# Kernel optimization log

Hardware: AMD Instinct MI355X
Metric: run time of the kernel (lower is better)

## Reference

```python
import jax, jax.numpy as jnp
import numpy as np

N_HEAD = 16
N_FEAT = 1024
D_HEAD = N_FEAT // N_HEAD


def setup_inputs() -> dict:
    key = jax.random.key(0)
    ks = jax.random.split(key, 12)
    B, L, T = 8, 128, 64
    s = 0.05
    return {
        "q": jax.random.normal(ks[0], (B, 1, N_FEAT), jnp.float32),
        "kv": jax.random.normal(ks[1], (B, L, T, N_FEAT), jnp.float32),
        "Wq": jax.random.normal(ks[2], (D_HEAD, D_HEAD), jnp.float32) * s,
        "bq": jax.random.normal(ks[3], (D_HEAD,), jnp.float32) * s,
        "Wk": jax.random.normal(ks[4], (D_HEAD, D_HEAD), jnp.float32) * s,
        "bk": jax.random.normal(ks[5], (D_HEAD,), jnp.float32) * s,
        "Wv": jax.random.normal(ks[6], (D_HEAD, D_HEAD), jnp.float32) * s,
        "bv": jax.random.normal(ks[7], (D_HEAD,), jnp.float32) * s,
        "Wo": jax.random.normal(ks[8], (N_FEAT, N_FEAT), jnp.float32) * s,
        "bo": jax.random.normal(ks[9], (N_FEAT,), jnp.float32) * s,
    }


def reference(q, kv, Wq, bq, Wk, bk, Wv, bv, Wo, bo):
    B, L, T, D = kv.shape
    H, dh = N_HEAD, D_HEAD
    # mean-pool q over its singleton length dim and kv over T for keys
    qm = q.mean(axis=-2)                      # [B, D]
    km = kv.mean(axis=-2)                     # [B, L, D]
    qh = qm.reshape(B, H, dh)                 # [B, H, dh]
    kh = km.reshape(B, L, H, dh)              # [B, L, H, dh]
    vh = kv.reshape(B, L, T, H, dh)           # [B, L, T, H, dh]
    # per-head linear projections (torch Linear: x @ W.T + b)
    qh = qh @ Wq.T + bq
    kh = kh @ Wk.T + bk
    vh = vh @ Wv.T + bv
    # faithful transpose chain from the original module
    qh = jnp.swapaxes(qh, -2, -3)             # [H, B, dh]  (3D: swaps B and H)
    kh = jnp.swapaxes(kh, -2, -3)             # [B, H, L, dh]
    # broadcasted matmul -> cross-batch attention [B, H, B, L]
    attw = jnp.matmul(qh, jnp.swapaxes(kh, -1, -2)) / jnp.sqrt(jnp.float32(dh))
    attn = jax.nn.softmax(attw, axis=-1)      # [B, H, B, L]
    # value reshuffle: [B,L,T,H,dh] -> [B,H,T,L,dh] -> [B,H,T,dh,L] -> [B,H,T*dh,L]
    v = jnp.swapaxes(vh, -2, -4)
    v = jnp.swapaxes(v, -1, -2)
    v = v.reshape(B, H, T * dh, L)
    ct = jnp.matmul(attn, jnp.swapaxes(v, -1, -2))   # [B, H, B, T*dh]
    ct = ct.reshape(B, H, B, T, dh)
    ct = jnp.swapaxes(ct, -2, -4)                    # [B, T, B, H, dh]
    ct = ct.reshape(B, T, B, H * dh)                 # [B, T, B, D]
    return ct @ Wo.T + bo
```

## Files before the change

### kernel.cpp

```cpp
#include <hip/hip_runtime.h>
#include <hip/hip_bf16.h>

#define BDIM 8
#define LDIM 128
#define TDIM 64
#define NFEAT 1024
#define HNUM 16
#define DH 64

#define GM 4096
#define GN 1024
#define GK 1024

typedef __attribute__((ext_vector_type(8))) short short8;
typedef __attribute__((ext_vector_type(4))) float f32x4;

__device__ __forceinline__ unsigned short f2bf(float x) {
  union { float f; unsigned u; } v; v.f = x;
  unsigned r = v.u + 0x7fffu + ((v.u >> 16) & 1u);
  return (unsigned short)(r >> 16);
}

__device__ __forceinline__ void gload_lds16(const void* g, void* l) {
  __builtin_amdgcn_global_load_lds((const __attribute__((address_space(1))) void*)g,
                                   (__attribute__((address_space(3))) void*)l, 16, 0, 0);
}

__global__ __launch_bounds__(256) void mean_kernel(const float* __restrict__ kv,
                                                   float* __restrict__ km) {
  const int bl = blockIdx.x;
  const float* src = kv + (size_t)bl * (TDIM * NFEAT) + threadIdx.x * 4;
  float4 acc = make_float4(0.f, 0.f, 0.f, 0.f);
#pragma unroll 4
  for (int t = 0; t < TDIM; ++t) {
    const float4 v = *(const float4*)(src + t * NFEAT);
    acc.x += v.x; acc.y += v.y; acc.z += v.z; acc.w += v.w;
  }
  const float s = 1.f / TDIM;
  const float4 o = make_float4(acc.x * s, acc.y * s, acc.z * s, acc.w * s);
  *(float4*)(km + (size_t)bl * NFEAT + threadIdx.x * 4) = o;
}

__global__ __launch_bounds__(128) void attn_kernel(const float* __restrict__ q,
                                                   const float* __restrict__ km,
                                                   const float* __restrict__ Wq,
                                                   const float* __restrict__ bq,
                                                   const float* __restrict__ Wk,
                                                   float* __restrict__ attn) {
  __shared__ float qp_s[BDIM * DH];
  __shared__ float qk_s[BDIM * DH];
  __shared__ float sw[BDIM * LDIM];
  __shared__ float mred[BDIM], ired[BDIM];
  const int b1 = blockIdx.x;
  const int h  = blockIdx.y;
  const int tid = threadIdx.x;

  {
    const int e0 = tid * 4;
    const int b2 = e0 >> 6;
    const int d0 = e0 & 63;
    float a0 = bq[d0], a1 = bq[d0 + 1], a2 = bq[d0 + 2], a3 = bq[d0 + 3];
    const float* qrow = q + b2 * NFEAT + h * DH;
#pragma unroll 4
    for (int i = 0; i < DH; ++i) {
      const float qv = qrow[i];
      a0 += qv * Wq[(d0 + 0) * DH + i];
      a1 += qv * Wq[(d0 + 1) * DH + i];
      a2 += qv * Wq[(d0 + 2) * DH + i];
      a3 += qv * Wq[(d0 + 3) * DH + i];
    }
    qp_s[e0 + 0] = a0; qp_s[e0 + 1] = a1; qp_s[e0 + 2] = a2; qp_s[e0 + 3] = a3;
  }
  __syncthreads();
  {
    const int e0 = tid * 4;
    const int b2 = e0 >> 6;
    const int i0 = e0 & 63;
    float a0 = 0, a1 = 0, a2 = 0, a3 = 0;
#pragma unroll 4
    for (int d = 0; d < DH; ++d) {
      const float qpv = qp_s[b2 * DH + d];
      const float4 wk4 = *(const float4*)(Wk + d * DH + i0);
      a0 += qpv * wk4.x; a1 += qpv * wk4.y; a2 += qpv * wk4.z; a3 += qpv * wk4.w;
    }
    qk_s[e0 + 0] = a0; qk_s[e0 + 1] = a1; qk_s[e0 + 2] = a2; qk_s[e0 + 3] = a3;
  }
  __syncthreads();
  const int l = tid;
  {
    const float* kmrow = km + (size_t)(b1 * LDIM + l) * NFEAT + h * DH;
    float s[8] = {0, 0, 0, 0, 0, 0, 0, 0};
#pragma unroll
    for (int i4 = 0; i4 < DH / 4; ++i4) {
      const float4 kmv = *(const float4*)(kmrow + i4 * 4);
#pragma unroll
      for (int b2 = 0; b2 < 8; ++b2) {
        const float4 qk4 = *(const float4*)(qk_s + b2 * DH + i4 * 4);
        s[b2] += kmv.x * qk4.x + kmv.y * qk4.y + kmv.z * qk4.z + kmv.w * qk4.w;
      }
    }
#pragma unroll
    for (int b2 = 0; b2 < 8; ++b2) sw[b2 * LDIM + l] = s[b2] * 0.125f;
  }
  __syncthreads();
  if (tid < 8) {
    const int b2 = tid;
    float m = -1e30f;
    for (int j = 0; j < LDIM; ++j) m = fmaxf(m, sw[b2 * LDIM + j]);
    float ssum = 0.f;
    for (int j = 0; j < LDIM; ++j) ssum += expf(sw[b2 * LDIM + j] - m);
    mred[b2] = m;
    ired[b2] = 1.f / ssum;
  }
  __syncthreads();
  float* abase = attn + ((size_t)(b1 * HNUM + h) * BDIM) * LDIM + l;
#pragma unroll
  for (int b2 = 0; b2 < 8; ++b2) {
    abase[b2 * LDIM] = expf(sw[b2 * LDIM + l] - mred[b2]) * ired[b2];
  }
}

__global__ __launch_bounds__(256) void weff_kernel(const float* __restrict__ Wo,
                                                   const float* __restrict__ Wv,
                                                   const float* __restrict__ bv,
                                                   const float* __restrict__ bo,
                                                   unsigned short* __restrict__ Weff,
                                                   float* __restrict__ beff) {
  __shared__ float worow[NFEAT];
  __shared__ float red[256];
  const int f = blockIdx.x;
  const int tid = threadIdx.x;
  *(float4*)(worow + tid * 4) = *(const float4*)(Wo + (size_t)f * NFEAT + tid * 4);
  __syncthreads();
  const int g0 = tid * 4;
  const int hbase = (g0 >> 6) << 6;
  const int i0 = g0 & 63;
  float a0 = 0, a1 = 0, a2 = 0, a3 = 0;
#pragma unroll 4
  for (int d = 0; d < DH; ++d) {
    const float wod = worow[hbase + d];
    const float4 wv4 = *(const float4*)(Wv + d * DH + i0);
    a0 += wod * wv4.x; a1 += wod * wv4.y; a2 += wod * wv4.z; a3 += wod * wv4.w;
  }
  ushort4 pk;
  pk.x = f2bf(a0); pk.y = f2bf(a1); pk.z = f2bf(a2); pk.w = f2bf(a3);
  *(ushort4*)(Weff + (size_t)f * NFEAT + g0) = pk;
  red[tid] = worow[g0 + 0] * bv[i0 + 0] + worow[g0 + 1] * bv[i0 + 1] +
             worow[g0 + 2] * bv[i0 + 2] + worow[g0 + 3] * bv[i0 + 3];
  __syncthreads();
  for (int sft = 128; sft > 0; sft >>= 1) {
    if (tid < sft) red[tid] += red[tid + sft];
    __syncthreads();
  }
  if (tid == 0) beff[f] = bo[f] + red[0];
}

__global__ __launch_bounds__(64) void pool_kernel(const float* __restrict__ kv,
                                                  const float* __restrict__ attn,
                                                  unsigned short* __restrict__ pooled) {
  __shared__ float wlds[4 * BDIM * LDIM];
  const int b1 = blockIdx.x;
  const int t = blockIdx.y;
  const int ftile = blockIdx.z;
  const int tid = threadIdx.x;
  {
    const float* src = attn + ((size_t)(b1 * HNUM + ftile * 4)) * (BDIM * LDIM);
#pragma unroll
    for (int j = 0; j < 16; ++j) {
      const int idx = (j * 64 + tid) * 4;
      *(float4*)(wlds + idx) = *(const float4*)(src + idx);
    }
  }
  __syncthreads();
  const int f = ftile * 256 + tid * 4;
  const int hh = tid >> 4;
  const float* kvbase = kv + ((size_t)b1 * LDIM) * (TDIM * NFEAT) + t * NFEAT + f;
  float4 acc[8];
#pragma unroll
  for (int b2 = 0; b2 < 8; ++b2) acc[b2] = make_float4(0.f, 0.f, 0.f, 0.f);
  const float* wbase = wlds + hh * (BDIM * LDIM);
#pragma unroll 2
  for (int l = 0; l < LDIM; ++l) {
    const float4 v = *(const float4*)(kvbase + (size_t)l * (TDIM * NFEAT));
#pragma unroll
    for (int b2 = 0; b2 < 8; ++b2) {
      const float w = wbase[b2 * LDIM + l];
      acc[b2].x += w * v.x; acc[b2].y += w * v.y;
      acc[b2].z += w * v.z; acc[b2].w += w * v.w;
    }
  }
  unsigned short* obase = pooled + ((size_t)(b1 * TDIM + t) * BDIM) * NFEAT + f;
#pragma unroll
  for (int b2 = 0; b2 < 8; ++b2) {
    ushort4 pk;
    pk.x = f2bf(acc[b2].x); pk.y = f2bf(acc[b2].y);
    pk.z = f2bf(acc[b2].z); pk.w = f2bf(acc[b2].w);
    *(ushort4*)(obase + b2 * NFEAT) = pk;
  }
}

__global__ __launch_bounds__(256) void mfma_gemm(const unsigned short* __restrict__ A,
                                                 const unsigned short* __restrict__ W,
                                                 const float* __restrict__ beff,
                                                 float* __restrict__ out) {
  __shared__ unsigned short As[128 * 32];
  __shared__ unsigned short Bs[128 * 32];
  const int tid = threadIdx.x;
  const int w = tid >> 6, l = tid & 63;
  const int mBase = blockIdx.y * 128, nBase = blockIdx.x * 128;
  const int wr = w >> 1, wc = w & 1;

  int sr[2], sc[2];
#pragma unroll
  for (int j = 0; j < 2; ++j) {
    const int o = (w * 2 + j) * 1024 + l * 16;
    const int r = o >> 6;
    const int c = (o >> 4) & 3;
    sr[j] = r;
    sc[j] = (c ^ ((r >> 1) & 3)) * 8;
  }
  const int rl = l & 15, ks = l >> 4;
  const int fsel = (ks ^ ((rl >> 1) & 3)) * 16;
  const int aoff0 = (wr * 64 + rl) * 64 + fsel;
  const int boff0 = (wc * 64 + rl) * 64 + fsel;

  f32x4 acc[4][4] = {};
  for (int k0 = 0; k0 < GK; k0 += 32) {
#pragma unroll
    for (int j = 0; j < 2; ++j) {
      gload_lds16(A + (size_t)(mBase + sr[j]) * GK + k0 + sc[j],
                  (char*)As + (w * 2 + j) * 1024);
      gload_lds16(W + (size_t)(nBase + sr[j]) * GK + k0 + sc[j],
                  (char*)Bs + (w * 2 + j) * 1024);
    }
    __syncthreads();
    short8 a[4], b[4];
#pragma unroll
    for (int m = 0; m < 4; ++m)
      a[m] = *(const short8*)((const char*)As + aoff0 + m * 1024);
#pragma unroll
    for (int n = 0; n < 4; ++n)
      b[n] = *(const short8*)((const char*)Bs + boff0 + n * 1024);
#pragma unroll
    for (int m = 0; m < 4; ++m)
#pragma unroll
      for (int n = 0; n < 4; ++n)
        acc[m][n] = __builtin_amdgcn_mfma_f32_16x16x32_bf16(a[m], b[n], acc[m][n], 0, 0, 0);
    __syncthreads();
  }

#pragma unroll
  for (int n = 0; n < 4; ++n) {
    const int col = nBase + wc * 64 + n * 16 + rl;
    const float bv = beff[col];
#pragma unroll
    for (int m = 0; m < 4; ++m) {
      const int row0 = mBase + wr * 64 + m * 16 + ks * 4;
#pragma unroll
      for (int j2 = 0; j2 < 4; ++j2)
        out[(size_t)(row0 + j2) * GN + col] = acc[m][n][j2] + bv;
    }
  }
}

extern "C" void kernel_launch(void* const* d_in, const int* in_sizes, int n_in,
                              void* d_out, int out_size, void* d_ws, size_t ws_size,
                              hipStream_t stream) {
  const float* q  = (const float*)d_in[0];
  const float* kv = (const float*)d_in[1];
  const float* Wq = (const float*)d_in[2];
  const float* bq = (const float*)d_in[3];
  const float* Wk = (const float*)d_in[4];
  const float* Wv = (const float*)d_in[6];
  const float* bv = (const float*)d_in[7];
  const float* Wo = (const float*)d_in[8];
  const float* bo = (const float*)d_in[9];
  float* out = (float*)d_out;

  char* ws = (char*)d_ws;
  float*          km     = (float*)ws;
  float*          attn   = (float*)(ws + (4u << 20));
  float*          beff   = (float*)(ws + (4u << 20) + (512u << 10));
  unsigned short* Weff   = (unsigned short*)(ws + (4u << 20) + (516u << 10));
  unsigned short* pooled = (unsigned short*)(ws + (4u << 20) + (516u << 10) + (2u << 20));

  mean_kernel<<<BDIM * LDIM, 256, 0, stream>>>(kv, km);
  attn_kernel<<<dim3(BDIM, HNUM), 128, 0, stream>>>(q, km, Wq, bq, Wk, attn);
  weff_kernel<<<NFEAT, 256, 0, stream>>>(Wo, Wv, bv, bo, Weff, beff);
  pool_kernel<<<dim3(BDIM, TDIM, 4), 64, 0, stream>>>(kv, attn, pooled);
  mfma_gemm<<<dim3(GN / 128, GM / 128), 256, 0, stream>>>(pooled, Weff, beff, out);
}
```

Baseline: 153.7 us.

## Batch loads in mean/pool kernels, pad LDS, double-buffer narrower GEMM tiles

```diff
diff --git a/kernel.cpp b/kernel.cpp
--- a/kernel.cpp
+++ b/kernel.cpp
@@ -31,10 +31,14 @@
   const int bl = blockIdx.x;
   const float* src = kv + (size_t)bl * (TDIM * NFEAT) + threadIdx.x * 4;
   float4 acc = make_float4(0.f, 0.f, 0.f, 0.f);
-#pragma unroll 4
-  for (int t = 0; t < TDIM; ++t) {
-    const float4 v = *(const float4*)(src + t * NFEAT);
-    acc.x += v.x; acc.y += v.y; acc.z += v.z; acc.w += v.w;
+  for (int t0 = 0; t0 < TDIM; t0 += 8) {
+    float4 v[8];
+#pragma unroll
+    for (int j = 0; j < 8; ++j) v[j] = *(const float4*)(src + (t0 + j) * NFEAT);
+#pragma unroll
+    for (int j = 0; j < 8; ++j) {
+      acc.x += v[j].x; acc.y += v[j].y; acc.z += v[j].z; acc.w += v[j].w;
+    }
   }
   const float s = 1.f / TDIM;
   const float4 o = make_float4(acc.x * s, acc.y * s, acc.z * s, acc.w * s);
@@ -155,20 +159,24 @@
   if (tid == 0) beff[f] = bo[f] + red[0];
 }
 
+#define HSTRIDE 1032
 __global__ __launch_bounds__(64) void pool_kernel(const float* __restrict__ kv,
                                                   const float* __restrict__ attn,
                                                   unsigned short* __restrict__ pooled) {
-  __shared__ float wlds[4 * BDIM * LDIM];
+  __shared__ float wlds[4 * HSTRIDE];
   const int b1 = blockIdx.x;
   const int t = blockIdx.y;
   const int ftile = blockIdx.z;
   const int tid = threadIdx.x;
   {
-    const float* src = attn + ((size_t)(b1 * HNUM + ftile * 4)) * (BDIM * LDIM);
-#pragma unroll
-    for (int j = 0; j < 16; ++j) {
-      const int idx = (j * 64 + tid) * 4;
-      *(float4*)(wlds + idx) = *(const float4*)(src + idx);
+#pragma unroll
+    for (int hg = 0; hg < 4; ++hg) {
+      const float* src = attn + ((size_t)(b1 * HNUM + ftile * 4 + hg)) * (BDIM * LDIM);
+#pragma unroll
+      for (int j = 0; j < 4; ++j) {
+        const int idx = (j * 64 + tid) * 4;
+        *(float4*)(wlds + hg * HSTRIDE + idx) = *(const float4*)(src + idx);
+      }
     }
   }
   __syncthreads();
@@ -178,15 +186,20 @@
   float4 acc[8];
 #pragma unroll
   for (int b2 = 0; b2 < 8; ++b2) acc[b2] = make_float4(0.f, 0.f, 0.f, 0.f);
-  const float* wbase = wlds + hh * (BDIM * LDIM);
-#pragma unroll 2
-  for (int l = 0; l < LDIM; ++l) {
-    const float4 v = *(const float4*)(kvbase + (size_t)l * (TDIM * NFEAT));
-#pragma unroll
-    for (int b2 = 0; b2 < 8; ++b2) {
-      const float w = wbase[b2 * LDIM + l];
-      acc[b2].x += w * v.x; acc[b2].y += w * v.y;
-      acc[b2].z += w * v.z; acc[b2].w += w * v.w;
+  const float* wbase = wlds + hh * HSTRIDE;
+  for (int l0 = 0; l0 < LDIM; l0 += 8) {
+    float4 v[8];
+#pragma unroll
+    for (int j = 0; j < 8; ++j)
+      v[j] = *(const float4*)(kvbase + (size_t)(l0 + j) * (TDIM * NFEAT));
+#pragma unroll
+    for (int j = 0; j < 8; ++j) {
+#pragma unroll
+      for (int b2 = 0; b2 < 8; ++b2) {
+        const float w = wbase[b2 * LDIM + l0 + j];
+        acc[b2].x += w * v[j].x; acc[b2].y += w * v[j].y;
+        acc[b2].z += w * v[j].z; acc[b2].w += w * v[j].w;
+      }
     }
   }
   unsigned short* obase = pooled + ((size_t)(b1 * TDIM + t) * BDIM) * NFEAT + f;
@@ -203,55 +216,66 @@
                                                  const unsigned short* __restrict__ W,
                                                  const float* __restrict__ beff,
                                                  float* __restrict__ out) {
-  __shared__ unsigned short As[128 * 32];
-  __shared__ unsigned short Bs[128 * 32];
+  __shared__ unsigned short As[2][128 * 32];
+  __shared__ unsigned short Bs[2][64 * 32];
   const int tid = threadIdx.x;
   const int w = tid >> 6, l = tid & 63;
-  const int mBase = blockIdx.y * 128, nBase = blockIdx.x * 128;
+  const int mBase = blockIdx.y * 128, nBase = blockIdx.x * 64;
   const int wr = w >> 1, wc = w & 1;
 
-  int sr[2], sc[2];
+  int arow[2], acol[2];
 #pragma unroll
   for (int j = 0; j < 2; ++j) {
-    const int o = (w * 2 + j) * 1024 + l * 16;
-    const int r = o >> 6;
-    const int c = (o >> 4) & 3;
-    sr[j] = r;
-    sc[j] = (c ^ ((r >> 1) & 3)) * 8;
-  }
+    const int cid = j * 256 + tid;
+    const int r = cid >> 2, c = cid & 3;
+    arow[j] = r;
+    acol[j] = (c ^ ((r >> 1) & 3)) * 8;
+  }
+  const int brow = tid >> 2;
+  const int bcol = ((tid & 3) ^ ((brow >> 1) & 3)) * 8;
+
   const int rl = l & 15, ks = l >> 4;
   const int fsel = (ks ^ ((rl >> 1) & 3)) * 16;
-  const int aoff0 = (wr * 64 + rl) * 64 + fsel;
-  const int boff0 = (wc * 64 + rl) * 64 + fsel;
-
-  f32x4 acc[4][4] = {};
-  for (int k0 = 0; k0 < GK; k0 += 32) {
-#pragma unroll
-    for (int j = 0; j < 2; ++j) {
-      gload_lds16(A + (size_t)(mBase + sr[j]) * GK + k0 + sc[j],
-                  (char*)As + (w * 2 + j) * 1024);
-      gload_lds16(W + (size_t)(nBase + sr[j]) * GK + k0 + sc[j],
-                  (char*)Bs + (w * 2 + j) * 1024);
-    }
-    __syncthreads();
-    short8 a[4], b[4];
+
+  f32x4 acc[4][2] = {};
+
+#pragma unroll
+  for (int j = 0; j < 2; ++j)
+    gload_lds16(A + (size_t)(mBase + arow[j]) * GK + acol[j],
+                (char*)As[0] + (j * 256 + tid) * 16);
+  gload_lds16(W + (size_t)(nBase + brow) * GK + bcol, (char*)Bs[0] + tid * 16);
+  __syncthreads();
+
+  int cur = 0;
+  for (int t = 0; t < GK / 32; ++t) {
+    if (t + 1 < GK / 32) {
+      const int k0 = (t + 1) * 32;
+#pragma unroll
+      for (int j = 0; j < 2; ++j)
+        gload_lds16(A + (size_t)(mBase + arow[j]) * GK + k0 + acol[j],
+                    (char*)As[cur ^ 1] + (j * 256 + tid) * 16);
+      gload_lds16(W + (size_t)(nBase + brow) * GK + k0 + bcol,
+                  (char*)Bs[cur ^ 1] + tid * 16);
+    }
+    short8 a[4], b[2];
 #pragma unroll
     for (int m = 0; m < 4; ++m)
-      a[m] = *(const short8*)((const char*)As + aoff0 + m * 1024);
-#pragma unroll
-    for (int n = 0; n < 4; ++n)
-      b[n] = *(const short8*)((const char*)Bs + boff0 + n * 1024);
+      a[m] = *(const short8*)((const char*)As[cur] + (wr * 64 + m * 16 + rl) * 64 + fsel);
+#pragma unroll
+    for (int n = 0; n < 2; ++n)
+      b[n] = *(const short8*)((const char*)Bs[cur] + (wc * 32 + n * 16 + rl) * 64 + fsel);
 #pragma unroll
     for (int m = 0; m < 4; ++m)
 #pragma unroll
-      for (int n = 0; n < 4; ++n)
+      for (int n = 0; n < 2; ++n)
         acc[m][n] = __builtin_amdgcn_mfma_f32_16x16x32_bf16(a[m], b[n], acc[m][n], 0, 0, 0);
     __syncthreads();
-  }
-
-#pragma unroll
-  for (int n = 0; n < 4; ++n) {
-    const int col = nBase + wc * 64 + n * 16 + rl;
+    cur ^= 1;
+  }
+
+#pragma unroll
+  for (int n = 0; n < 2; ++n) {
+    const int col = nBase + wc * 32 + n * 16 + rl;
     const float bv = beff[col];
 #pragma unroll
     for (int m = 0; m < 4; ++m) {
@@ -284,9 +308,9 @@
   unsigned short* Weff   = (unsigned short*)(ws + (4u << 20) + (516u << 10));
   unsigned short* pooled = (unsigned short*)(ws + (4u << 20) + (516u << 10) + (2u << 20));
 
+  weff_kernel<<<NFEAT, 256, 0, stream>>>(Wo, Wv, bv, bo, Weff, beff);
   mean_kernel<<<BDIM * LDIM, 256, 0, stream>>>(kv, km);
   attn_kernel<<<dim3(BDIM, HNUM), 128, 0, stream>>>(q, km, Wq, bq, Wk, attn);
-  weff_kernel<<<NFEAT, 256, 0, stream>>>(Wo, Wv, bv, bo, Weff, beff);
   pool_kernel<<<dim3(BDIM, TDIM, 4), 64, 0, stream>>>(kv, attn, pooled);
-  mfma_gemm<<<dim3(GN / 128, GM / 128), 256, 0, stream>>>(pooled, Weff, beff, out);
-}
+  mfma_gemm<<<dim3(GN / 64, GM / 128), 256, 0, stream>>>(pooled, Weff, beff, out);
+}
```

Result: faster. 147.9 us (-3.7%).
